# Performance work log

Hardware: AMD Instinct MI355X
Metric: run time of the kernel (lower is better)

## Reference

```python
import jax, jax.numpy as jnp
import numpy as np

N, D_MODEL, D_PE, H = 4096, 512, 16, 8


def setup_inputs() -> dict:
    key = jax.random.key(0)
    ks = jax.random.split(key, 6)
    s = 1.0 / np.sqrt(D_MODEL)
    return {
        "x": jax.random.normal(ks[0], (N, D_MODEL), dtype=jnp.float32),
        "pe": jax.random.normal(ks[1], (N, D_PE), dtype=jnp.float32),
        "w_qkv": jax.random.normal(ks[2], (D_MODEL, 3 * D_MODEL), dtype=jnp.float32) * s,
        "b_qkv": jnp.zeros((3 * D_MODEL,), dtype=jnp.float32),
        "w_pe": jax.random.normal(ks[3], (D_PE, H), dtype=jnp.float32) * (1.0 / np.sqrt(D_PE)),
        "b_pe": jnp.zeros((H,), dtype=jnp.float32),
        "w_out": jax.random.normal(ks[4], (D_MODEL, D_MODEL), dtype=jnp.float32) * s,
        "b_out": jnp.zeros((D_MODEL,), dtype=jnp.float32),
    }


def reference(x, pe, w_qkv, b_qkv, w_pe, b_pe, w_out, b_out):
    n, d = x.shape
    h = w_pe.shape[1]
    hd = d // h
    scale = hd ** -0.5

    qkv = (x @ w_qkv + b_qkv).reshape(n, 3, h, hd)  # [N,3,H,hd]
    q = jnp.transpose(qkv[:, 0], (1, 0, 2))  # [H,N,hd]
    k = jnp.transpose(qkv[:, 1], (1, 0, 2))
    v = jnp.transpose(qkv[:, 2], (1, 0, 2))

    pe_proj = pe @ w_pe + b_pe  # [N,H]
    # bias[h,i,j] = pe_proj[j,h] - pe_proj[i,h]  (matches torch unsqueeze/permute)
    pt = pe_proj.T  # [H,N]
    bias = pt[:, None, :] - pt[:, :, None]  # [H,N,N]

    scores = jnp.einsum('hnd,hmd->hnm', q, k) * scale + bias  # [H,N,N]
    attn = jax.nn.softmax(scores, axis=-1)
    out = jnp.einsum('hnm,hmd->hnd', attn, v)  # [H,N,hd]
    out = jnp.transpose(out, (1, 0, 2)).reshape(n, d)
    return out @ w_out + b_out
```

## Files before the change

### kernel.cpp

```cpp
#include <hip/hip_runtime.h>
#include <stdint.h>
#include <stddef.h>


typedef unsigned short u16;
typedef __attribute__((ext_vector_type(8))) short short8;
typedef __attribute__((ext_vector_type(8))) unsigned short us8;
typedef __attribute__((ext_vector_type(4))) unsigned short us4;
typedef __attribute__((ext_vector_type(4))) float floatx4;

__device__ __forceinline__ u16 f2b(float f) {
  union { float f; uint32_t u; } v; v.f = f;
  uint32_t u = v.u;
  return (u16)((u + 0x7fffu + ((u >> 16) & 1u)) >> 16);
}

__device__ __forceinline__ uint32_t pkbf16(float a, float b) {
  union { float f; uint32_t u; } x, y; x.f = a; y.f = b;
  return __builtin_amdgcn_perm(y.u + 0x8000u, x.u + 0x8000u, 0x07060302u);
}

#if __has_builtin(__builtin_amdgcn_exp2f)
__device__ __forceinline__ float fexp2(float x) { return __builtin_amdgcn_exp2f(x); }
#else
__device__ __forceinline__ float fexp2(float x) { return exp2f(x); }
#endif

__device__ __forceinline__ void gld16(const u16* g, u16* l) {
  __builtin_amdgcn_global_load_lds(
      (const __attribute__((address_space(1))) uint32_t*)(const void*)g,
      (__attribute__((address_space(3))) uint32_t*)(void*)l, 16, 0, 0);
}


__device__ __forceinline__ void tr_tile(const float* __restrict__ in,
                                        u16* __restrict__ out, int R, int C,
                                        int bx, int by, u16 (*tile)[33]) {
  int tx = threadIdx.x & 31, ty = threadIdx.x >> 5;
  int c0 = bx * 32, r0 = by * 32;
#pragma unroll
  for (int i = 0; i < 32; i += 8)
    tile[ty + i][tx] = f2b(in[(size_t)(r0 + ty + i) * C + c0 + tx]);
  __syncthreads();
#pragma unroll
  for (int i = 0; i < 32; i += 8)
    out[(size_t)(c0 + ty + i) * R + r0 + tx] = tile[tx][ty + i];
}

__global__ __launch_bounds__(256) void k_prep(
    const float* __restrict__ x, u16* __restrict__ xb,
    const float* __restrict__ w_qkv, u16* __restrict__ wqkvT,
    const float* __restrict__ w_out, u16* __restrict__ woutT,
    const float* __restrict__ pe, const float* __restrict__ w_pe,
    const float* __restrict__ b_pe, float* __restrict__ wexp,
    u16* __restrict__ wpb) {
  __shared__ u16 tile[32][33];
  int b = blockIdx.x;
  if (b < 2048) {
    int i = b * 256 + threadIdx.x;
    float4 v = ((const float4*)x)[i];
    uint2 o = make_uint2(pkbf16(v.x, v.y), pkbf16(v.z, v.w));
    ((uint2*)xb)[i] = o;
  } else if (b < 2816) {
    int idx = b - 2048;
    tr_tile(w_qkv, wqkvT, 512, 1536, idx % 48, idx / 48, tile);
  } else if (b < 3072) {
    int idx = b - 2816;
    tr_tile(w_out, woutT, 512, 512, idx % 16, idx / 16, tile);
  } else {
    int idx = (b - 3072) * 256 + threadIdx.x;
    int h = idx >> 12, n = idx & 4095;
    float acc = b_pe[h];
#pragma unroll
    for (int d = 0; d < 16; ++d) acc = fmaf(pe[n * 16 + d], w_pe[d * 8 + h], acc);
    float w = exp2f(acc * 1.4426950408889634f - 16.0f);
    u16 wb = f2b(w);
    union { uint32_t u; float f; } cv; cv.u = ((uint32_t)wb) << 16;
    wexp[h * 4096 + n] = cv.f;
    int pn = (n & ~31) | (((n >> 2) & 3) << 3) | (((n >> 4) & 1) << 2) | (n & 3);
    wpb[h * 4096 + pn] = wb;
  }
}


__global__ __launch_bounds__(512, 6) void k_gemm_qkv(const u16* __restrict__ A,
                                                     const u16* __restrict__ Bt,
                                                     const float* __restrict__ bias,
                                                     const float* __restrict__ wexp,
                                                     u16* __restrict__ qk,
                                                     u16* __restrict__ vtp) {
  __shared__ __align__(16) u16 smem[24576];
  const int tid = threadIdx.x;
  const int lane = tid & 63, wave = tid >> 6;
  const int colx = lane & 15, quad = lane >> 4;
  const int m0 = blockIdx.y * 64, n0 = blockIdx.x * 128;
  const int wm = wave >> 2, wn = wave & 3;
  const int sc = (lane & 7) ^ ((lane >> 3) & 7);
  const floatx4 fz = {0.f, 0.f, 0.f, 0.f};
  floatx4 acc[2][2];
#pragma unroll
  for (int i = 0; i < 2; ++i)
#pragma unroll
    for (int j = 0; j < 2; ++j) acc[i][j] = fz;

#define PREF_QKV(k0, b)                                                       \
  {                                                                           \
    int rowa = wave * 8 + (lane >> 3);                                        \
    gld16(&A[(size_t)(m0 + rowa) * 512 + (k0) + sc * 8],                      \
          &smem[(b) * 4096 + wave * 512 + lane * 8]);                         \
    _Pragma("unroll") for (int c = 0; c < 2; ++c) {                           \
      int rowb = wave * 16 + c * 8 + (lane >> 3);                             \
      gld16(&Bt[(size_t)(n0 + rowb) * 512 + (k0) + sc * 8],                   \
            &smem[8192 + (b) * 8192 + wave * 1024 + c * 512 + lane * 8]);     \
    }                                                                         \
  }

  PREF_QKV(0, 0);
  __syncthreads();
  for (int it = 0; it < 8; ++it) {
    int cur = it & 1;
    if (it < 7) PREF_QKV((it + 1) * 64, cur ^ 1);
    const u16* As = &smem[cur * 4096];
    const u16* Bs = &smem[8192 + cur * 8192];
#pragma unroll
    for (int kk = 0; kk < 2; ++kk) {
      short8 af[2], bf[2];
#pragma unroll
      for (int i = 0; i < 2; ++i) {
        int row = wm * 32 + i * 16 + colx;
        af[i] = *(const short8*)&As[row * 64 + (((kk * 4 + quad) ^ (colx & 7))) * 8];
      }
#pragma unroll
      for (int j = 0; j < 2; ++j) {
        int row = wn * 32 + j * 16 + colx;
        bf[j] = *(const short8*)&Bs[row * 64 + (((kk * 4 + quad) ^ (colx & 7))) * 8];
      }
#pragma unroll
      for (int i = 0; i < 2; ++i)
#pragma unroll
        for (int j = 0; j < 2; ++j)
          acc[i][j] = __builtin_amdgcn_mfma_f32_16x16x32_bf16(af[i], bf[j], acc[i][j], 0, 0, 0);
    }
    __syncthreads();
  }

  const bool isV = (blockIdx.x >= 8);
  if (!isV) {
#pragma unroll
    for (int j = 0; j < 2; ++j) {
      int c = n0 + wn * 32 + j * 16 + colx;
      float bq = bias[c];
      float qs = (c < 512) ? 0.18033688011112042f : 1.0f;
#pragma unroll
      for (int i = 0; i < 2; ++i)
#pragma unroll
        for (int r = 0; r < 4; ++r) {
          int row = m0 + wm * 32 + i * 16 + quad * 4 + r;
          qk[(size_t)row * 1024 + c] = f2b((acc[i][j][r] + bq) * qs);
        }
    }
  } else {
    const int dv = n0 - 1024;
    u16* Vl = smem;
    const int hh = (dv + wn * 32) >> 6;
#pragma unroll
    for (int j = 0; j < 2; ++j) {
      float bq = bias[n0 + wn * 32 + j * 16 + colx];
#pragma unroll
      for (int i = 0; i < 2; ++i) {
        floatx4 wv = *(const floatx4*)&wexp[hh * 4096 + m0 + wm * 32 + i * 16 + quad * 4];
        us4 o;
#pragma unroll
        for (int r = 0; r < 4; ++r) o[r] = f2b((acc[i][j][r] + bq) * wv[r]);
        int dl = wn * 32 + j * 16 + colx;
        int nc = wm * 32 + quad * 8 + i * 4;
        *(us4*)&Vl[dl * 72 + nc] = o;
      }
    }
    __syncthreads();
#pragma unroll
    for (int t = 0; t < 2; ++t) {
      int idx = t * 512 + tid;
      int dl = idx >> 3, ch = idx & 7;
      *(us8*)&vtp[(size_t)(dv + dl) * 4096 + m0 + ch * 8] =
          *(const us8*)&Vl[dl * 72 + ch * 8];
    }
  }
#undef PREF_QKV
}


__global__ __launch_bounds__(512, 8) void k_flash(const u16* __restrict__ qk,
                                                  const u16* __restrict__ vt,
                                                  const u16* __restrict__ wpb,
                                                  float* __restrict__ opart,
                                                  float* __restrict__ lpart) {
  __shared__ __align__(16) u16 smem[20480];
  float* bufs = (float*)smem;

  const int tid = threadIdx.x;
  const int lane = tid & 63, wave = tid >> 6;
  const int colx = lane & 15, quad = lane >> 4;
  const int ih = wave >> 1, jq = wave & 1;
  const int q0 = blockIdx.x * 64;
  const int h = blockIdx.y;
  const int z = blockIdx.z;
  const int kvb = z * 2048;
  const floatx4 fz = {0.f, 0.f, 0.f, 0.f};

  const int sc = (lane & 7) ^ ((lane >> 3) & 7);
  const int srow = wave * 8 + (lane >> 3);

  {
    int row = tid >> 3, ch = tid & 7;
    *(us8*)&smem[row * 64 + (ch ^ (row & 7)) * 8] =
        *(const us8*)&qk[(size_t)(q0 + row) * 1024 + h * 64 + ch * 8];
  }
  const u16* qptr = qk + (size_t)(kvb + srow) * 1024 + 512 + h * 64 + sc * 8;
  const u16* vptr = vt + (size_t)(h * 64 + srow) * 4096 + kvb + sc * 8;
  const u16* wptr = wpb + h * 4096 + kvb + jq * 32 + quad * 8;
  gld16(qptr, &smem[4096 + wave * 512 + lane * 8]);
  gld16(vptr, &smem[12288 + wave * 512 + lane * 8]);
  qptr += 65536;
  vptr += 64;
  __syncthreads();

  short8 qf[2];
#pragma unroll
  for (int kk = 0; kk < 2; ++kk) {
    int row = ih * 16 + colx;
    qf[kk] = *(const short8*)&smem[row * 64 + (((kk * 4 + quad) ^ (colx & 7))) * 8];
  }

  floatx4 oacc[4], lacc = fz;
#pragma unroll
  for (int cb = 0; cb < 4; ++cb) oacc[cb] = fz;

#define FBODY(CUR, PREF)                                                      \
  {                                                                           \
    short8 wf = *(const short8*)wptr;                                         \
    wptr += 64;                                                               \
    if (PREF) {                                                               \
      gld16(qptr, &smem[4096 + (1 - (CUR)) * 4096 + wave * 512 + lane * 8]);  \
      gld16(vptr, &smem[12288 + (1 - (CUR)) * 4096 + wave * 512 + lane * 8]); \
      qptr += 65536;                                                          \
      vptr += 64;                                                             \
    }                                                                         \
    const u16* Ks = &smem[4096 + (CUR) * 4096];                               \
    const u16* Vts = &smem[12288 + (CUR) * 4096];                             \
    floatx4 sacc[2] = {fz, fz};                                               \
    _Pragma("unroll") for (int j2 = 0; j2 < 2; ++j2) {                        \
      _Pragma("unroll") for (int kk = 0; kk < 2; ++kk) {                      \
        int row = jq * 32 + j2 * 16 + colx;                                   \
        short8 kf = *(const short8*)&Ks[row * 64 +                            \
                                        (((kk * 4 + quad) ^ (colx & 7))) * 8];\
        sacc[j2] =                                                            \
            __builtin_amdgcn_mfma_f32_16x16x32_bf16(kf, qf[kk], sacc[j2], 0, 0, 0); \
      }                                                                       \
    }                                                                         \
    union { uint32_t w[4]; short8 s; } pk;                                    \
    _Pragma("unroll") for (int j2 = 0; j2 < 2; ++j2) {                        \
      float p0 = fexp2(sacc[j2][0]);                                          \
      float p1 = fexp2(sacc[j2][1]);                                          \
      float p2 = fexp2(sacc[j2][2]);                                          \
      float p3 = fexp2(sacc[j2][3]);                                          \
      pk.w[j2 * 2 + 0] = pkbf16(p0, p1);                                      \
      pk.w[j2 * 2 + 1] = pkbf16(p2, p3);                                      \
    }                                                                         \
    _Pragma("unroll") for (int cb = 0; cb < 4; ++cb) {                        \
      int row = cb * 16 + colx;                                               \
      short8 vf = *(const short8*)&Vts[row * 64 +                             \
                                       (((jq * 4 + quad) ^ (colx & 7))) * 8]; \
      oacc[cb] =                                                              \
          __builtin_amdgcn_mfma_f32_16x16x32_bf16(pk.s, vf, oacc[cb], 0, 0, 0); \
    }                                                                         \
    lacc = __builtin_amdgcn_mfma_f32_16x16x32_bf16(pk.s, wf, lacc, 0, 0, 0);  \
    __syncthreads();                                                          \
  }

  for (int t = 0; t < 15; ++t) {
    FBODY(0, 1)
    FBODY(1, 1)
  }
  FBODY(0, 1)
  FBODY(1, 0)
#undef FBODY

  float* b = bufs + ih * 1040;
  if (jq == 1) {
#pragma unroll
    for (int cb = 0; cb < 4; ++cb)
#pragma unroll
      for (int r = 0; r < 4; ++r)
        b[(quad * 4 + r) * 65 + cb * 16 + colx] = oacc[cb][r];
    if (colx == 0)
#pragma unroll
      for (int r = 0; r < 4; ++r) b[(quad * 4 + r) * 65 + 64] = lacc[r];
  }
  __syncthreads();
  if (jq == 0) {
#pragma unroll
    for (int cb = 0; cb < 4; ++cb)
#pragma unroll
      for (int r = 0; r < 4; ++r)
        oacc[cb][r] += b[(quad * 4 + r) * 65 + cb * 16 + colx];
#pragma unroll
    for (int r = 0; r < 4; ++r) lacc[r] += b[(quad * 4 + r) * 65 + 64];
    float* op = opart + (size_t)z * 2097152;
#pragma unroll
    for (int cb = 0; cb < 4; ++cb)
#pragma unroll
      for (int r = 0; r < 4; ++r)
        op[(size_t)(q0 + ih * 16 + quad * 4 + r) * 512 + h * 64 + cb * 16 + colx] =
            oacc[cb][r];
    if (colx == 0)
#pragma unroll
      for (int r = 0; r < 4; ++r)
        lpart[z * 32768 + h * 4096 + q0 + ih * 16 + quad * 4 + r] = lacc[r];
  }
}


__global__ __launch_bounds__(256) void k_comb(const float* __restrict__ opart,
                                              const float* __restrict__ lpart,
                                              u16* __restrict__ ao) {
  int idx = blockIdx.x * 256 + threadIdx.x;
  int n = idx >> 7, d4 = idx & 127;
  int h = d4 >> 4;
  float l = lpart[h * 4096 + n] + lpart[32768 + h * 4096 + n];
  float inv = 1.0f / l;
  float4 o0 = *(const float4*)&opart[(size_t)n * 512 + d4 * 4];
  float4 o1 = *(const float4*)&opart[2097152 + (size_t)n * 512 + d4 * 4];
  us4 o;
  o[0] = f2b((o0.x + o1.x) * inv);
  o[1] = f2b((o0.y + o1.y) * inv);
  o[2] = f2b((o0.z + o1.z) * inv);
  o[3] = f2b((o0.w + o1.w) * inv);
  *(us4*)&ao[(size_t)n * 512 + d4 * 4] = o;
}


__global__ __launch_bounds__(512, 4) void k_gemm_out(const u16* __restrict__ A,
                                                     const u16* __restrict__ Bt,
                                                     const float* __restrict__ bias,
                                                     float* __restrict__ Cout) {
  __shared__ __align__(16) u16 smem[16384];
  const int tid = threadIdx.x;
  const int lane = tid & 63, wave = tid >> 6;
  const int colx = lane & 15, quad = lane >> 4;
  const int m0 = blockIdx.y * 64, n0 = blockIdx.x * 64;
  const int wm = wave >> 2, wn = wave & 3;
  const int sc = (lane & 7) ^ ((lane >> 3) & 7);
  const floatx4 fz = {0.f, 0.f, 0.f, 0.f};
  floatx4 acc[2];
  acc[0] = fz; acc[1] = fz;

#define PREF_OUT(k0, b)                                                       \
  {                                                                           \
    int rowa = wave * 8 + (lane >> 3);                                        \
    gld16(&A[(size_t)(m0 + rowa) * 512 + (k0) + sc * 8],                      \
          &smem[(b) * 4096 + wave * 512 + lane * 8]);                         \
    gld16(&Bt[(size_t)(n0 + rowa) * 512 + (k0) + sc * 8],                     \
          &smem[8192 + (b) * 4096 + wave * 512 + lane * 8]);                  \
  }

  PREF_OUT(0, 0);
  __syncthreads();
  for (int it = 0; it < 8; ++it) {
    int cur = it & 1;
    if (it < 7) PREF_OUT((it + 1) * 64, cur ^ 1);
    const u16* As = &smem[cur * 4096];
    const u16* Bs = &smem[8192 + cur * 4096];
#pragma unroll
    for (int kk = 0; kk < 2; ++kk) {
      short8 af[2], bf;
#pragma unroll
      for (int i = 0; i < 2; ++i) {
        int row = wm * 32 + i * 16 + colx;
        af[i] = *(const short8*)&As[row * 64 + (((kk * 4 + quad) ^ (colx & 7))) * 8];
      }
      {
        int row = wn * 16 + colx;
        bf = *(const short8*)&Bs[row * 64 + (((kk * 4 + quad) ^ (colx & 7))) * 8];
      }
#pragma unroll
      for (int i = 0; i < 2; ++i)
        acc[i] = __builtin_amdgcn_mfma_f32_16x16x32_bf16(af[i], bf, acc[i], 0, 0, 0);
    }
    __syncthreads();
  }
  int c = n0 + wn * 16 + colx;
  float bq = bias[c];
#pragma unroll
  for (int i = 0; i < 2; ++i)
#pragma unroll
    for (int r = 0; r < 4; ++r) {
      int row = m0 + wm * 32 + i * 16 + quad * 4 + r;
      Cout[(size_t)row * 512 + c] = acc[i][r] + bq;
    }
#undef PREF_OUT
}


extern "C" void kernel_launch(void* const* d_in, const int* in_sizes, int n_in,
                              void* d_out, int out_size, void* d_ws, size_t ws_size,
                              hipStream_t stream) {
  const float* x     = (const float*)d_in[0];
  const float* pe    = (const float*)d_in[1];
  const float* w_qkv = (const float*)d_in[2];
  const float* b_qkv = (const float*)d_in[3];
  const float* w_pe  = (const float*)d_in[4];
  const float* b_pe  = (const float*)d_in[5];
  const float* w_out = (const float*)d_in[6];
  const float* b_out = (const float*)d_in[7];
  float* out = (float*)d_out;

  u16* xb    = (u16*)d_ws;
  u16* wqkvT = xb    + 2097152;
  u16* woutT = wqkvT + 786432;
  u16* qk    = woutT + 262144;
  u16* vt    = qk    + 4194304;
  u16* wpb   = vt    + 2097152;
  u16* ao    = wpb   + 32768;
  float* wexp  = (float*)(ao + 2097152);
  float* opart = wexp + 32768;
  float* lpart = opart + 4194304;

  k_prep<<<3200, 256, 0, stream>>>(x, xb, w_qkv, wqkvT, w_out, woutT,
                                   pe, w_pe, b_pe, wexp, wpb);
  k_gemm_qkv<<<dim3(12, 64), 512, 0, stream>>>(xb, wqkvT, b_qkv, wexp, qk, vt);
  k_flash<<<dim3(64, 8, 2), 512, 0, stream>>>(qk, vt, wpb, opart, lpart);
  k_comb<<<2048, 256, 0, stream>>>(opart, lpart, ao);
  k_gemm_out<<<dim3(8, 64), 512, 0, stream>>>(ao, woutT, b_out, out);
}
```

Measured before the change: 143.7 us.

## Halve flash block threads, each wave computes two query row tiles

```diff
diff --git a/kernel.cpp b/kernel.cpp
--- a/kernel.cpp
+++ b/kernel.cpp
@@ -190,7 +190,7 @@
 }
 
 
-__global__ __launch_bounds__(512, 8) void k_flash(const u16* __restrict__ qk,
+__global__ __launch_bounds__(256, 4) void k_flash(const u16* __restrict__ qk,
                                                   const u16* __restrict__ vt,
                                                   const u16* __restrict__ wpb,
                                                   float* __restrict__ opart,
@@ -209,72 +209,92 @@
   const floatx4 fz = {0.f, 0.f, 0.f, 0.f};
 
   const int sc = (lane & 7) ^ ((lane >> 3) & 7);
-  const int srow = wave * 8 + (lane >> 3);
-
-  {
-    int row = tid >> 3, ch = tid & 7;
+  const int srow = wave * 16 + (lane >> 3);
+
+#pragma unroll
+  for (int t = 0; t < 2; ++t) {
+    int idx = t * 256 + tid;
+    int row = idx >> 3, ch = idx & 7;
     *(us8*)&smem[row * 64 + (ch ^ (row & 7)) * 8] =
         *(const us8*)&qk[(size_t)(q0 + row) * 1024 + h * 64 + ch * 8];
   }
   const u16* qptr = qk + (size_t)(kvb + srow) * 1024 + 512 + h * 64 + sc * 8;
   const u16* vptr = vt + (size_t)(h * 64 + srow) * 4096 + kvb + sc * 8;
   const u16* wptr = wpb + h * 4096 + kvb + jq * 32 + quad * 8;
-  gld16(qptr, &smem[4096 + wave * 512 + lane * 8]);
-  gld16(vptr, &smem[12288 + wave * 512 + lane * 8]);
+  gld16(qptr, &smem[4096 + wave * 1024 + lane * 8]);
+  gld16(qptr + 8192, &smem[4096 + wave * 1024 + 512 + lane * 8]);
+  gld16(vptr, &smem[12288 + wave * 1024 + lane * 8]);
+  gld16(vptr + 32768, &smem[12288 + wave * 1024 + 512 + lane * 8]);
   qptr += 65536;
   vptr += 64;
   __syncthreads();
 
-  short8 qf[2];
-#pragma unroll
-  for (int kk = 0; kk < 2; ++kk) {
-    int row = ih * 16 + colx;
-    qf[kk] = *(const short8*)&smem[row * 64 + (((kk * 4 + quad) ^ (colx & 7))) * 8];
-  }
-
-  floatx4 oacc[4], lacc = fz;
-#pragma unroll
-  for (int cb = 0; cb < 4; ++cb) oacc[cb] = fz;
+  short8 qf[2][2];
+#pragma unroll
+  for (int iq = 0; iq < 2; ++iq)
+#pragma unroll
+    for (int kk = 0; kk < 2; ++kk) {
+      int row = ih * 32 + iq * 16 + colx;
+      qf[iq][kk] = *(const short8*)&smem[row * 64 + (((kk * 4 + quad) ^ (colx & 7))) * 8];
+    }
+
+  floatx4 oacc[2][4], lacc[2];
+  lacc[0] = fz; lacc[1] = fz;
+#pragma unroll
+  for (int iq = 0; iq < 2; ++iq)
+#pragma unroll
+    for (int cb = 0; cb < 4; ++cb) oacc[iq][cb] = fz;
 
 #define FBODY(CUR, PREF)                                                      \
   {                                                                           \
     short8 wf = *(const short8*)wptr;                                         \
     wptr += 64;                                                               \
     if (PREF) {                                                               \
-      gld16(qptr, &smem[4096 + (1 - (CUR)) * 4096 + wave * 512 + lane * 8]);  \
-      gld16(vptr, &smem[12288 + (1 - (CUR)) * 4096 + wave * 512 + lane * 8]); \
+      gld16(qptr, &smem[4096 + (1 - (CUR)) * 4096 + wave * 1024 + lane * 8]); \
+      gld16(qptr + 8192,                                                      \
+            &smem[4096 + (1 - (CUR)) * 4096 + wave * 1024 + 512 + lane * 8]); \
+      gld16(vptr, &smem[12288 + (1 - (CUR)) * 4096 + wave * 1024 + lane * 8]);\
+      gld16(vptr + 32768,                                                     \
+            &smem[12288 + (1 - (CUR)) * 4096 + wave * 1024 + 512 + lane * 8]);\
       qptr += 65536;                                                          \
       vptr += 64;                                                             \
     }                                                                         \
     const u16* Ks = &smem[4096 + (CUR) * 4096];                               \
     const u16* Vts = &smem[12288 + (CUR) * 4096];                             \
-    floatx4 sacc[2] = {fz, fz};                                               \
+    floatx4 sacc[2][2] = {{fz, fz}, {fz, fz}};                                \
     _Pragma("unroll") for (int j2 = 0; j2 < 2; ++j2) {                        \
       _Pragma("unroll") for (int kk = 0; kk < 2; ++kk) {                      \
         int row = jq * 32 + j2 * 16 + colx;                                   \
         short8 kf = *(const short8*)&Ks[row * 64 +                            \
                                         (((kk * 4 + quad) ^ (colx & 7))) * 8];\
-        sacc[j2] =                                                            \
-            __builtin_amdgcn_mfma_f32_16x16x32_bf16(kf, qf[kk], sacc[j2], 0, 0, 0); \
+        sacc[0][j2] = __builtin_amdgcn_mfma_f32_16x16x32_bf16(                \
+            kf, qf[0][kk], sacc[0][j2], 0, 0, 0);                             \
+        sacc[1][j2] = __builtin_amdgcn_mfma_f32_16x16x32_bf16(                \
+            kf, qf[1][kk], sacc[1][j2], 0, 0, 0);                             \
       }                                                                       \
     }                                                                         \
-    union { uint32_t w[4]; short8 s; } pk;                                    \
-    _Pragma("unroll") for (int j2 = 0; j2 < 2; ++j2) {                        \
-      float p0 = fexp2(sacc[j2][0]);                                          \
-      float p1 = fexp2(sacc[j2][1]);                                          \
-      float p2 = fexp2(sacc[j2][2]);                                          \
-      float p3 = fexp2(sacc[j2][3]);                                          \
-      pk.w[j2 * 2 + 0] = pkbf16(p0, p1);                                      \
-      pk.w[j2 * 2 + 1] = pkbf16(p2, p3);                                      \
+    union { uint32_t w[4]; short8 s; } pk[2];                                 \
+    _Pragma("unroll") for (int iq = 0; iq < 2; ++iq) {                        \
+      _Pragma("unroll") for (int j2 = 0; j2 < 2; ++j2) {                      \
+        float p0 = fexp2(sacc[iq][j2][0]);                                    \
+        float p1 = fexp2(sacc[iq][j2][1]);                                    \
+        float p2 = fexp2(sacc[iq][j2][2]);                                    \
+        float p3 = fexp2(sacc[iq][j2][3]);                                    \
+        pk[iq].w[j2 * 2 + 0] = pkbf16(p0, p1);                                \
+        pk[iq].w[j2 * 2 + 1] = pkbf16(p2, p3);                                \
+      }                                                                       \
     }                                                                         \
     _Pragma("unroll") for (int cb = 0; cb < 4; ++cb) {                        \
       int row = cb * 16 + colx;                                               \
       short8 vf = *(const short8*)&Vts[row * 64 +                             \
                                        (((jq * 4 + quad) ^ (colx & 7))) * 8]; \
-      oacc[cb] =                                                              \
-          __builtin_amdgcn_mfma_f32_16x16x32_bf16(pk.s, vf, oacc[cb], 0, 0, 0); \
+      oacc[0][cb] = __builtin_amdgcn_mfma_f32_16x16x32_bf16(                  \
+          pk[0].s, vf, oacc[0][cb], 0, 0, 0);                                 \
+      oacc[1][cb] = __builtin_amdgcn_mfma_f32_16x16x32_bf16(                  \
+          pk[1].s, vf, oacc[1][cb], 0, 0, 0);                                 \
     }                                                                         \
-    lacc = __builtin_amdgcn_mfma_f32_16x16x32_bf16(pk.s, wf, lacc, 0, 0, 0);  \
+    lacc[0] = __builtin_amdgcn_mfma_f32_16x16x32_bf16(pk[0].s, wf, lacc[0], 0, 0, 0); \
+    lacc[1] = __builtin_amdgcn_mfma_f32_16x16x32_bf16(pk[1].s, wf, lacc[1], 0, 0, 0); \
     __syncthreads();                                                          \
   }
 
@@ -286,37 +306,48 @@
   FBODY(1, 0)
 #undef FBODY
 
-  float* b = bufs + ih * 1040;
+  float* b = bufs + ih * 2080;
   if (jq == 1) {
 #pragma unroll
-    for (int cb = 0; cb < 4; ++cb)
-#pragma unroll
-      for (int r = 0; r < 4; ++r)
-        b[(quad * 4 + r) * 65 + cb * 16 + colx] = oacc[cb][r];
+    for (int iq = 0; iq < 2; ++iq)
+#pragma unroll
+      for (int cb = 0; cb < 4; ++cb)
+#pragma unroll
+        for (int r = 0; r < 4; ++r)
+          b[(iq * 16 + quad * 4 + r) * 65 + cb * 16 + colx] = oacc[iq][cb][r];
     if (colx == 0)
 #pragma unroll
-      for (int r = 0; r < 4; ++r) b[(quad * 4 + r) * 65 + 64] = lacc[r];
+      for (int iq = 0; iq < 2; ++iq)
+#pragma unroll
+        for (int r = 0; r < 4; ++r) b[(iq * 16 + quad * 4 + r) * 65 + 64] = lacc[iq][r];
   }
   __syncthreads();
   if (jq == 0) {
 #pragma unroll
-    for (int cb = 0; cb < 4; ++cb)
-#pragma unroll
-      for (int r = 0; r < 4; ++r)
-        oacc[cb][r] += b[(quad * 4 + r) * 65 + cb * 16 + colx];
-#pragma unroll
-    for (int r = 0; r < 4; ++r) lacc[r] += b[(quad * 4 + r) * 65 + 64];
+    for (int iq = 0; iq < 2; ++iq) {
+#pragma unroll
+      for (int cb = 0; cb < 4; ++cb)
+#pragma unroll
+        for (int r = 0; r < 4; ++r)
+          oacc[iq][cb][r] += b[(iq * 16 + quad * 4 + r) * 65 + cb * 16 + colx];
+#pragma unroll
+      for (int r = 0; r < 4; ++r) lacc[iq][r] += b[(iq * 16 + quad * 4 + r) * 65 + 64];
+    }
     float* op = opart + (size_t)z * 2097152;
 #pragma unroll
-    for (int cb = 0; cb < 4; ++cb)
-#pragma unroll
-      for (int r = 0; r < 4; ++r)
-        op[(size_t)(q0 + ih * 16 + quad * 4 + r) * 512 + h * 64 + cb * 16 + colx] =
-            oacc[cb][r];
+    for (int iq = 0; iq < 2; ++iq)
+#pragma unroll
+      for (int cb = 0; cb < 4; ++cb)
+#pragma unroll
+        for (int r = 0; r < 4; ++r)
+          op[(size_t)(q0 + ih * 32 + iq * 16 + quad * 4 + r) * 512 + h * 64 + cb * 16 + colx] =
+              oacc[iq][cb][r];
     if (colx == 0)
 #pragma unroll
-      for (int r = 0; r < 4; ++r)
-        lpart[z * 32768 + h * 4096 + q0 + ih * 16 + quad * 4 + r] = lacc[r];
+      for (int iq = 0; iq < 2; ++iq)
+#pragma unroll
+        for (int r = 0; r < 4; ++r)
+          lpart[z * 32768 + h * 4096 + q0 + ih * 32 + iq * 16 + quad * 4 + r] = lacc[iq][r];
   }
 }
 
@@ -429,7 +460,7 @@
   k_prep<<<3200, 256, 0, stream>>>(x, xb, w_qkv, wqkvT, w_out, woutT,
                                    pe, w_pe, b_pe, wexp, wpb);
   k_gemm_qkv<<<dim3(12, 64), 512, 0, stream>>>(xb, wqkvT, b_qkv, wexp, qk, vt);
-  k_flash<<<dim3(64, 8, 2), 512, 0, stream>>>(qk, vt, wpb, opart, lpart);
+  k_flash<<<dim3(64, 8, 2), 256, 0, stream>>>(qk, vt, wpb, opart, lpart);
   k_comb<<<2048, 256, 0, stream>>>(opart, lpart, ao);
   k_gemm_out<<<dim3(8, 64), 512, 0, stream>>>(ao, woutT, b_out, out);
 }
```

Measured after the change: 143.8 us. About the same (+0.1%).
